# Performance work log

Measured on AMD Instinct MI355X. Metric: run time of the kernel, lower is better.

Reference implementation:

```python
import jax, jax.numpy as jnp
import numpy as np

DIM = 3072
HEADS = 24
HD = 128  # head_dim
RANK = 64
COND = 1024      # (512//8)*(512//8)*16//64
BLOCK = 2048     # main latent tokens
SEQ = BLOCK + COND
NIP = 64         # image_emb tokens
LORA_W = 1.0     # lora_weights[0]
ALPHA_SCALE = 1.0  # network_alpha / rank = 64/64
IP_SCALE = 1.0


def setup_inputs() -> dict:
    key = jax.random.key(0)
    ks = jax.random.split(key, 21)
    d = {}
    d["hidden_states"] = jax.random.normal(ks[0], (1, SEQ, DIM), jnp.float32)
    d["image_emb"] = jax.random.normal(ks[1], (1, NIP, DIM), jnp.float32)
    d["rope_cos"] = jax.random.uniform(ks[2], (SEQ, HD), jnp.float32)
    d["rope_sin"] = jax.random.uniform(ks[3], (SEQ, HD), jnp.float32)
    d["wq"] = jax.random.normal(ks[4], (DIM, DIM), jnp.float32) * 0.02
    d["bq"] = jax.random.normal(ks[5], (DIM,), jnp.float32) * 0.02
    d["wk"] = jax.random.normal(ks[6], (DIM, DIM), jnp.float32) * 0.02
    d["bk"] = jax.random.normal(ks[7], (DIM,), jnp.float32) * 0.02
    d["wv"] = jax.random.normal(ks[8], (DIM, DIM), jnp.float32) * 0.02
    d["bv"] = jax.random.normal(ks[9], (DIM,), jnp.float32) * 0.02
    d["norm_q_w"] = jax.random.uniform(ks[10], (HD,), jnp.float32, 0.5, 1.5)
    d["norm_k_w"] = jax.random.uniform(ks[11], (HD,), jnp.float32, 0.5, 1.5)
    d["q_down"] = jax.random.normal(ks[12], (RANK, DIM), jnp.float32) / RANK
    d["q_up"] = jax.random.normal(ks[13], (DIM, RANK), jnp.float32) * 0.02
    d["k_down"] = jax.random.normal(ks[14], (RANK, DIM), jnp.float32) / RANK
    d["k_up"] = jax.random.normal(ks[15], (DIM, RANK), jnp.float32) * 0.02
    d["v_down"] = jax.random.normal(ks[16], (RANK, DIM), jnp.float32) / RANK
    d["v_up"] = jax.random.normal(ks[17], (DIM, RANK), jnp.float32) * 0.02
    d["wk_ip"] = jax.random.normal(ks[18], (DIM, DIM), jnp.float32) * 0.02
    d["wv_ip"] = jax.random.normal(ks[19], (DIM, DIM), jnp.float32) * 0.02
    return d


def _rmsnorm(x, w, eps):
    v = jnp.mean(jnp.square(x), axis=-1, keepdims=True)
    y = x * jax.lax.rsqrt(v + eps)
    return y if w is None else y * w


def _heads(x, b):  # (B,S,DIM) -> (B,H,S,HD)
    return x.reshape(b, -1, HEADS, HD).transpose(0, 2, 1, 3)


def _rope(x, cos, sin):
    # diffusers apply_rotary_emb, use_real, unbind_dim=-1
    x1 = x[..., 0::2]
    x2 = x[..., 1::2]
    rot = jnp.stack([-x2, x1], axis=-1).reshape(x.shape)
    return x * cos[None, None] + rot * sin[None, None]


def _sdpa(q, k, v, bias=None):
    s = jnp.einsum("bhqd,bhkd->bhqk", q, k) / jnp.sqrt(jnp.float32(q.shape[-1]))
    if bias is not None:
        s = s + bias
    p = jax.nn.softmax(s, axis=-1)
    return jnp.einsum("bhqk,bhkd->bhqd", p, v)


def reference(hidden_states, image_emb, rope_cos, rope_sin,
              wq, bq, wk, bk, wv, bv, norm_q_w, norm_k_w,
              q_down, q_up, k_down, k_up, v_down, v_up, wk_ip, wv_ip):
    B = hidden_states.shape[0]

    # base QKV projections
    q = hidden_states @ wq.T + bq
    k = hidden_states @ wk.T + bk
    v = hidden_states @ wv.T + bv

    # original (pre-LoRA, pre-norm, pre-RoPE) query on the main block for IP attention
    original_query = _heads(hidden_states[:, :BLOCK] @ wq.T + bq, B)

    # masked LoRA add (n_loras=1): only tokens [BLOCK, BLOCK+COND) contribute
    pos = jnp.arange(SEQ)
    tok_mask = ((pos >= BLOCK) & (pos < BLOCK + COND)).astype(hidden_states.dtype)
    hm = hidden_states * tok_mask[None, :, None]
    q = q + LORA_W * ALPHA_SCALE * ((hm @ q_down.T) @ q_up.T)
    k = k + LORA_W * ALPHA_SCALE * ((hm @ k_down.T) @ k_up.T)
    v = v + LORA_W * ALPHA_SCALE * ((hm @ v_down.T) @ v_up.T)

    q = _heads(q, B)
    k = _heads(k, B)
    v = _heads(v, B)

    # per-head RMSNorm (attn.norm_q / attn.norm_k, eps=1e-6 in Flux)
    q = _rmsnorm(q, norm_q_w, 1e-6)
    k = _rmsnorm(k, norm_k_w, 1e-6)

    # IP-adapter cross attention with the original query
    ip_k = _rmsnorm(_heads(image_emb @ wk_ip.T, B), None, 1e-5)
    ip_v = _heads(image_emb @ wv_ip.T, B)
    ip_out = _sdpa(original_query, ip_k, ip_v)  # (B,H,BLOCK,HD)
    ip_out = ip_out.transpose(0, 2, 1, 3).reshape(B, -1, DIM)

    # RoPE on q/k
    q = _rope(q, rope_cos, rope_sin)
    k = _rope(k, rope_cos, rope_sin)

    # attention bias: main-block queries see everything; cond queries only their own block
    m = jnp.ones((SEQ, SEQ), jnp.float32)
    m = m.at[:BLOCK, :].set(0.0)
    m = m.at[BLOCK:BLOCK + COND, BLOCK:BLOCK + COND].set(0.0)
    bias = (m * -1e20)[None, None]

    out = _sdpa(q, k, v, bias)  # (B,H,SEQ,HD)
    out = out.transpose(0, 2, 1, 3).reshape(B, SEQ, DIM)

    main = out[:, :BLOCK, :] + IP_SCALE * ip_out
    return main
```

## Files before the change

### kernel.cpp

```cpp
#include <hip/hip_runtime.h>
#include <stdint.h>

#define DIM 3072
#define HEADS 24
#define HD 128
#define RANKN 64
#define CONDN 1024
#define BLK 2048
#define SEQN 3072
#define NIPN 64

typedef __attribute__((ext_vector_type(8))) short s8v;
typedef __attribute__((ext_vector_type(4))) float fx4;

static __device__ __forceinline__ unsigned short f2bf(float f){
  union{float f; unsigned u;} v; v.f=f;
  unsigned r = v.u + 0x7FFFu + ((v.u>>16)&1u);
  return (unsigned short)(r>>16);
}

#define GL16(g,l) __builtin_amdgcn_global_load_lds((const __attribute__((address_space(1))) void*)(g), (__attribute__((address_space(3))) void*)(l), 16, 0, 0)
#define MFMA(a,b,c) __builtin_amdgcn_mfma_f32_16x16x32_bf16((a),(b),(c),0,0,0)

__global__ __launch_bounds__(256) void cvt_f32_bf16(const float* __restrict__ src,
                                                    unsigned short* __restrict__ dst, int n4){
  int i = blockIdx.x*256 + threadIdx.x;
  if (i < n4){
    float4 v = ((const float4*)src)[i];
    ushort4 o;
    o.x = f2bf(v.x); o.y = f2bf(v.y); o.z = f2bf(v.z); o.w = f2bf(v.w);
    ((ushort4*)dst)[i] = o;
  }
}

__global__ __launch_bounds__(256) void lora_down_g(const unsigned short* __restrict__ A,
                                                   const unsigned short* __restrict__ D0,
                                                   const unsigned short* __restrict__ D1,
                                                   unsigned short* __restrict__ outb){
  __shared__ unsigned short As[128*64];
  __shared__ unsigned short Bs[64*64];
  int tid = threadIdx.x, lane = tid & 63, w = tid >> 6;
  int l15 = lane & 15, l16 = lane >> 4;
  int z = blockIdx.z;
  int m0 = blockIdx.y * 128;
  const unsigned short* Dw = z ? D1 : D0;
  int wr = w * 32;
  fx4 acc[2][4] = {};
  for (int kt = 0; kt < DIM; kt += 64){
    #pragma unroll
    for (int i = 0; i < 4; i++){
      int p = i*256 + tid;
      int row = p >> 3, cc = p & 7;
      int gc = cc ^ (row & 7);
      GL16(A + (size_t)(m0+row)*DIM + kt + gc*8, As + p*8);
    }
    #pragma unroll
    for (int i = 0; i < 2; i++){
      int p = i*256 + tid;
      int row = p >> 3, cc = p & 7;
      int gc = cc ^ (row & 7);
      GL16(Dw + (size_t)row*DIM + kt + gc*8, Bs + p*8);
    }
    __syncthreads();
    #pragma unroll
    for (int kk = 0; kk < 2; kk++){
      s8v af[2], bfr[4];
      #pragma unroll
      for (int t = 0; t < 2; t++){
        int rowa = wr + t*16 + l15;
        int ca = (kk*4 + l16) ^ (rowa & 7);
        af[t] = *(const s8v*)(As + rowa*64 + ca*8);
      }
      #pragma unroll
      for (int t = 0; t < 4; t++){
        int rowb = t*16 + l15;
        int cb = (kk*4 + l16) ^ (rowb & 7);
        bfr[t] = *(const s8v*)(Bs + rowb*64 + cb*8);
      }
      #pragma unroll
      for (int mt = 0; mt < 2; mt++)
        #pragma unroll
        for (int nt = 0; nt < 4; nt++)
          acc[mt][nt] = MFMA(af[mt], bfr[nt], acc[mt][nt]);
    }
    __syncthreads();
  }
  #pragma unroll
  for (int mt = 0; mt < 2; mt++)
    #pragma unroll
    for (int j = 0; j < 4; j++){
      int row = m0 + wr + mt*16 + l16*4 + j;
      #pragma unroll
      for (int nt = 0; nt < 4; nt++){
        int col = nt*16 + l15;
        outb[((size_t)z*CONDN + row)*64 + col] = f2bf(acc[mt][nt][j]);
      }
    }
}

__global__ __launch_bounds__(512, 2) void gemm_256(
    const unsigned short* __restrict__ hs_bf,
    const unsigned short* __restrict__ ie_bf,
    const unsigned short* __restrict__ Wq,
    const unsigned short* __restrict__ Wk,
    const unsigned short* __restrict__ Wv,
    const unsigned short* __restrict__ Wik,
    const unsigned short* __restrict__ Wiv,
    const float* __restrict__ bq, const float* __restrict__ bk, const float* __restrict__ bv,
    const unsigned short* __restrict__ downb,
    const unsigned short* __restrict__ upk,
    const unsigned short* __restrict__ upv,
    float* __restrict__ qb, float* __restrict__ kb, float* __restrict__ vb,
    float* __restrict__ ipk_pre, float* __restrict__ ipv_pre)
{
  __shared__ unsigned short Ab[2][16384];
  __shared__ unsigned short Bb[2][16384];
  int tid = threadIdx.x, lane = tid & 63, w = tid >> 6;
  int wm = w >> 2, wn = w & 3;
  int l15 = lane & 15, l16 = lane >> 4;

  int b = blockIdx.x;
  int id = (b & 7) * 51 + (b >> 3);
  int z, mt, ntile;
  if (id < 96){ z = 0; mt = id / 12; ntile = id % 12; }
  else if (id < 240){ z = 1; int r = id - 96; mt = r / 12; ntile = r % 12; }
  else if (id < 384){ z = 2; int r = id - 240; mt = r / 12; ntile = r % 12; }
  else { z = 3; int r = id - 384; mt = r / 12; ntile = r % 12; }
  const bool is_ip = (z == 3);
  int z2 = is_ip ? mt : 0;
  int m0 = is_ip ? 0 : mt * 256;
  int n0 = ntile * 256;
  const unsigned short* A = is_ip ? ie_bf : hs_bf;
  const unsigned short* B = is_ip ? (z2 ? Wiv : Wik)
                                  : (z == 0 ? Wq : (z == 1 ? Wk : Wv));

  fx4 acc[8][4] = {};
  s8v af[8], bfr[8];

  auto stA = [&](int buf, int half, int kt){
    #pragma unroll
    for (int i = 0; i < 2; i++){
      int p = i*512 + tid;
      int row = p >> 3, cc = p & 7, gc = cc ^ (row & 7);
      int ar = m0 + half*128 + row;
      if (is_ip && ar > 63) ar = 63;
      GL16(A + (size_t)ar*DIM + kt + gc*8, &Ab[buf][half*8192 + p*8]);
    }
  };
  auto stB = [&](int buf, int half, int kt){
    #pragma unroll
    for (int i = 0; i < 2; i++){
      int p = i*512 + tid;
      int row = p >> 3, cc = p & 7, gc = cc ^ (row & 7);
      GL16(B + (size_t)(n0 + half*128 + row)*DIM + kt + gc*8, &Bb[buf][half*8192 + p*8]);
    }
  };
  auto rdA = [&](int buf, int m, int kk)->s8v{
    int rl = m*16 + l15;
    return *(const s8v*)(&Ab[buf][wm*8192 + rl*64 + ((kk*4 + l16) ^ (rl & 7))*8]);
  };
  auto rdB = [&](int buf, int n, int kk)->s8v{
    int rB = wn*64 + n*16 + l15;
    return *(const s8v*)(&Bb[buf][(rB >> 7)*8192 + (rB & 127)*64 + ((kk*4 + l16) ^ (rB & 7))*8]);
  };

  stA(0,0,0); stA(0,1,0); stB(0,0,0); stB(0,1,0);
  asm volatile("s_waitcnt vmcnt(0)" ::: "memory");
  __builtin_amdgcn_s_barrier();

  const int NT = DIM / 64;
  for (int t = 0; t < NT; t++){
    int cur = t & 1, nxt = cur ^ 1;
    int kt1 = (t + 1) * 64;
    bool pf = (t + 1 < NT);

    if (pf){
      stA(nxt, 0, kt1);
      asm volatile("s_waitcnt vmcnt(2)" ::: "memory");
    } else {
      asm volatile("s_waitcnt vmcnt(0)" ::: "memory");
    }
    __builtin_amdgcn_s_barrier();
    #pragma unroll
    for (int m = 0; m < 4; m++){ af[m*2] = rdA(cur,m,0); af[m*2+1] = rdA(cur,m,1); }
    #pragma unroll
    for (int n = 0; n < 2; n++){ bfr[n*2] = rdB(cur,n,0); bfr[n*2+1] = rdB(cur,n,1); }
    __builtin_amdgcn_s_setprio(1);
    #pragma unroll
    for (int m = 0; m < 4; m++)
      #pragma unroll
      for (int n = 0; n < 2; n++){
        acc[m][n] = MFMA(af[m*2],   bfr[n*2],   acc[m][n]);
        acc[m][n] = MFMA(af[m*2+1], bfr[n*2+1], acc[m][n]);
      }
    __builtin_amdgcn_s_setprio(0);
    __builtin_amdgcn_s_barrier();

    if (pf) stA(nxt, 1, kt1);
    #pragma unroll
    for (int n = 2; n < 4; n++){ bfr[n*2] = rdB(cur,n,0); bfr[n*2+1] = rdB(cur,n,1); }
    __builtin_amdgcn_s_setprio(1);
    #pragma unroll
    for (int m = 0; m < 4; m++)
      #pragma unroll
      for (int n = 2; n < 4; n++){
        acc[m][n] = MFMA(af[m*2],   bfr[n*2],   acc[m][n]);
        acc[m][n] = MFMA(af[m*2+1], bfr[n*2+1], acc[m][n]);
      }
    __builtin_amdgcn_s_setprio(0);
    __builtin_amdgcn_s_barrier();

    if (pf) stB(nxt, 0, kt1);
    #pragma unroll
    for (int m = 4; m < 8; m++){ af[(m-4)*2] = rdA(cur,m,0); af[(m-4)*2+1] = rdA(cur,m,1); }
    __builtin_amdgcn_s_setprio(1);
    #pragma unroll
    for (int m = 4; m < 8; m++)
      #pragma unroll
      for (int n = 2; n < 4; n++){
        acc[m][n] = MFMA(af[(m-4)*2],   bfr[n*2],   acc[m][n]);
        acc[m][n] = MFMA(af[(m-4)*2+1], bfr[n*2+1], acc[m][n]);
      }
    __builtin_amdgcn_s_setprio(0);
    __builtin_amdgcn_s_barrier();

    if (pf) stB(nxt, 1, kt1);
    __builtin_amdgcn_s_setprio(1);
    #pragma unroll
    for (int m = 4; m < 8; m++)
      #pragma unroll
      for (int n = 0; n < 2; n++){
        acc[m][n] = MFMA(af[(m-4)*2],   bfr[n*2],   acc[m][n]);
        acc[m][n] = MFMA(af[(m-4)*2+1], bfr[n*2+1], acc[m][n]);
      }
    __builtin_amdgcn_s_setprio(0);
    __builtin_amdgcn_s_barrier();
  }

  if (is_ip){
    float* outp = z2 ? ipv_pre : ipk_pre;
    if (wm == 0){
      #pragma unroll
      for (int m = 0; m < 4; m++)
        #pragma unroll
        for (int j = 0; j < 4; j++){
          int row = m*16 + l16*4 + j;
          #pragma unroll
          for (int n = 0; n < 4; n++)
            outp[(size_t)row*DIM + n0 + wn*64 + n*16 + l15] = acc[m][n][j];
        }
    }
    return;
  }

  if (z >= 1 && m0 >= BLK){
    const unsigned short* dwn = downb + (size_t)(z-1)*CONDN*64 + (size_t)(m0 - BLK)*64;
    const unsigned short* up  = (z == 1) ? upk : upv;
    #pragma unroll
    for (int i = 0; i < 4; i++){
      int p = i*512 + tid;
      int row = p >> 3, cc = p & 7, gc = cc ^ (row & 7);
      GL16(dwn + (size_t)row*64 + gc*8, &Ab[0][p*8]);
      GL16(up + (size_t)(n0 + row)*64 + gc*8, &Bb[0][p*8]);
    }
    asm volatile("s_waitcnt vmcnt(0)" ::: "memory");
    __builtin_amdgcn_s_barrier();
    #pragma unroll
    for (int kk = 0; kk < 2; kk++){
      s8v aL[8], bL[4];
      #pragma unroll
      for (int m = 0; m < 8; m++){
        int rA = wm*128 + m*16 + l15;
        aL[m] = *(const s8v*)(&Ab[0][rA*64 + ((kk*4 + l16) ^ (rA & 7))*8]);
      }
      #pragma unroll
      for (int n = 0; n < 4; n++){
        int rB = wn*64 + n*16 + l15;
        bL[n] = *(const s8v*)(&Bb[0][rB*64 + ((kk*4 + l16) ^ (rB & 7))*8]);
      }
      #pragma unroll
      for (int m = 0; m < 8; m++)
        #pragma unroll
        for (int n = 0; n < 4; n++)
          acc[m][n] = MFMA(aL[m], bL[n], acc[m][n]);
    }
  }

  {
    const float* bias = z == 0 ? bq : (z == 1 ? bk : bv);
    float* C = z == 0 ? qb : (z == 1 ? kb : vb);
    float bv4[4];
    #pragma unroll
    for (int n = 0; n < 4; n++) bv4[n] = bias[n0 + wn*64 + n*16 + l15];
    #pragma unroll
    for (int m = 0; m < 8; m++)
      #pragma unroll
      for (int j = 0; j < 4; j++){
        int row = m0 + wm*128 + m*16 + l16*4 + j;
        float* crow = C + (size_t)row*DIM;
        #pragma unroll
        for (int n = 0; n < 4; n++)
          crow[n0 + wn*64 + n*16 + l15] = acc[m][n][j] + bv4[n];
      }
  }
}

__global__ __launch_bounds__(256) void norm_rope(const float* __restrict__ src,
                                                 unsigned short* __restrict__ dst,
                                                 const float* __restrict__ wt,
                                                 const float* __restrict__ rc,
                                                 const float* __restrict__ rs,
                                                 int S, float qscale){
  int tid = threadIdx.x, lane = tid & 63, w = tid >> 6;
  int r = blockIdx.x*4 + w;
  int pos = r % S, h = r / S;
  const float* x = src + (size_t)pos*DIM + h*HD;
  float2 xv = *(const float2*)(x + 2*lane);
  float ss = xv.x*xv.x + xv.y*xv.y;
  #pragma unroll
  for (int o = 1; o < 64; o <<= 1) ss += __shfl_xor(ss, o);
  float rr = rsqrtf(ss*(1.f/128.f) + 1e-6f);
  float y0 = xv.x*rr*wt[2*lane], y1 = xv.y*rr*wt[2*lane+1];
  float2 cv = *(const float2*)(rc + (size_t)pos*HD + 2*lane);
  float2 sv = *(const float2*)(rs + (size_t)pos*HD + 2*lane);
  float o0 = (y0*cv.x - y1*sv.x)*qscale;
  float o1 = (y1*cv.y + y0*sv.y)*qscale;
  ushort2 ov; ov.x = f2bf(o0); ov.y = f2bf(o1);
  *(ushort2*)(dst + ((size_t)h*S + pos)*HD + 2*lane) = ov;
}

__global__ __launch_bounds__(256) void ipk_norm_bf(const float* __restrict__ src,
                                                   unsigned short* __restrict__ dst){
  int tid = threadIdx.x, lane = tid & 63, w = tid >> 6;
  int r = blockIdx.x*4 + w;
  int pos = r / HEADS, h = r % HEADS;
  const float* x = src + (size_t)pos*DIM + h*HD;
  float2 xv = *(const float2*)(x + 2*lane);
  float ss = xv.x*xv.x + xv.y*xv.y;
  #pragma unroll
  for (int o = 1; o < 64; o <<= 1) ss += __shfl_xor(ss, o);
  float rr = rsqrtf(ss*(1.f/128.f) + 1e-5f);
  ushort2 ov; ov.x = f2bf(xv.x*rr); ov.y = f2bf(xv.y*rr);
  *(ushort2*)(dst + ((size_t)h*NIPN + pos)*HD + 2*lane) = ov;
}

__global__ __launch_bounds__(256) void ipv_transpose(const float* __restrict__ ipv,
                                                     unsigned short* __restrict__ vt){
  int h = blockIdx.x, tid = threadIdx.x;
  #pragma unroll
  for (int i = 0; i < 32; i++){
    int idx = i*256 + tid;
    int d = idx >> 6, key = idx & 63;
    vt[((size_t)h*HD + d)*64 + key] = f2bf(ipv[(size_t)key*DIM + h*HD + d]);
  }
}

__global__ __launch_bounds__(256) void v_transpose(const float* __restrict__ v,
                                                   unsigned short* __restrict__ Vt){
  __shared__ float t[64][129];
  int h = blockIdx.y, p0 = blockIdx.x*64, tid = threadIdx.x;
  int dcol = tid & 127, prow2 = tid >> 7;
  #pragma unroll
  for (int i = 0; i < 32; i++){
    int pos = i*2 + prow2;
    t[pos][dcol] = v[(size_t)(p0+pos)*DIM + h*HD + dcol];
  }
  __syncthreads();
  int pos = tid & 63, dbase = tid >> 6;
  #pragma unroll
  for (int i = 0; i < 32; i++){
    int d = i*4 + dbase;
    Vt[((size_t)h*HD + d)*SEQN + p0 + pos] = f2bf(t[pos][d]);
  }
}

__global__ __launch_bounds__(256) void ip_attn_m(const float* __restrict__ qb,
                                                 const unsigned short* __restrict__ ipk_bf,
                                                 const unsigned short* __restrict__ ipv_t,
                                                 float* __restrict__ out){
  __shared__ unsigned short Ks[64*HD];
  __shared__ unsigned short Vs[HD*64];
  __shared__ unsigned short Ps[4][16*64];
  int tid = threadIdx.x, lane = tid & 63, w = tid >> 6;
  int l15 = lane & 15, l16 = lane >> 4;
  int h = blockIdx.y;
  int q0 = blockIdx.x*64 + w*16;
  const unsigned short* Kh = ipk_bf + (size_t)h*NIPN*HD;
  const unsigned short* Vh = ipv_t + (size_t)h*HD*NIPN;

  #pragma unroll
  for (int i = 0; i < 4; i++){
    int p = i*256 + tid;
    int row = p >> 4, cc = p & 15;
    int gc = cc ^ (row & 7);
    GL16(Kh + (size_t)row*HD + gc*8, Ks + p*8);
  }
  #pragma unroll
  for (int i = 0; i < 4; i++){
    int p = i*256 + tid;
    int row = p >> 3, cc = p & 7;
    int gc = cc ^ (row & 7);
    GL16(Vh + (size_t)row*64 + gc*8, Vs + p*8);
  }

  s8v qf[4];
  #pragma unroll
  for (int kf = 0; kf < 4; kf++){
    const float* qp = qb + (size_t)(q0 + l15)*DIM + h*HD + kf*32 + l16*8;
    float4 a = *(const float4*)qp;
    float4 b = *(const float4*)(qp + 4);
    s8v f;
    f[0]=(short)f2bf(a.x); f[1]=(short)f2bf(a.y); f[2]=(short)f2bf(a.z); f[3]=(short)f2bf(a.w);
    f[4]=(short)f2bf(b.x); f[5]=(short)f2bf(b.y); f[6]=(short)f2bf(b.z); f[7]=(short)f2bf(b.w);
    qf[kf] = f;
  }
  __syncthreads();

  fx4 s[4] = {};
  #pragma unroll
  for (int ct = 0; ct < 4; ct++){
    #pragma unroll
    for (int kk = 0; kk < 4; kk++){
      int row = ct*16 + l15;
      int c = (kk*4 + l16) ^ (row & 7);
      s8v b = *(const s8v*)(Ks + row*HD + c*8);
      s[ct] = MFMA(qf[kk], b, s[ct]);
    }
  }
  const float SC = 0.08838834764831845f;
  float lrow[4];
  #pragma unroll
  for (int j = 0; j < 4; j++){
    #pragma unroll
    for (int ct = 0; ct < 4; ct++) s[ct][j] *= SC;
    float v = fmaxf(fmaxf(s[0][j], s[1][j]), fmaxf(s[2][j], s[3][j]));
    #pragma unroll
    for (int o2 = 1; o2 < 16; o2 <<= 1) v = fmaxf(v, __shfl_xor(v, o2));
    float sum = 0.f;
    #pragma unroll
    for (int ct = 0; ct < 4; ct++){
      float p = __expf(s[ct][j] - v);
      s[ct][j] = p;
      sum += p;
    }
    #pragma unroll
    for (int o2 = 1; o2 < 16; o2 <<= 1) sum += __shfl_xor(sum, o2);
    lrow[j] = sum;
  }

  #pragma unroll
  for (int ct = 0; ct < 4; ct++)
    #pragma unroll
    for (int j = 0; j < 4; j++){
      int row = l16*4 + j;
      int cidx = ct*16 + l15;
      Ps[w][row*64 + (((cidx>>3) ^ (row&7))<<3) + (cidx&7)] = f2bf(s[ct][j]);
    }
  asm volatile("s_waitcnt lgkmcnt(0)" ::: "memory");
  s8v pa[2];
  #pragma unroll
  for (int kk = 0; kk < 2; kk++){
    int c = (kk*4 + l16) ^ (l15 & 7);
    pa[kk] = *(const s8v*)(&Ps[w][l15*64 + c*8]);
  }
  fx4 o[8] = {};
  #pragma unroll
  for (int nt = 0; nt < 8; nt++){
    #pragma unroll
    for (int kk = 0; kk < 2; kk++){
      int row = nt*16 + l15;
      int c = (kk*4 + l16) ^ (row & 7);
      s8v bv = *(const s8v*)(Vs + row*64 + c*8);
      o[nt] = MFMA(pa[kk], bv, o[nt]);
    }
  }
  #pragma unroll
  for (int nt = 0; nt < 8; nt++)
    #pragma unroll
    for (int j = 0; j < 4; j++){
      int row = q0 + l16*4 + j;
      int d = nt*16 + l15;
      out[(size_t)row*DIM + h*HD + d] = o[nt][j] / lrow[j];
    }
}

#define QB 128
#define KVB 64
#define PSTR 72
__global__ __launch_bounds__(512, 4) void flash_attn_split(const unsigned short* __restrict__ Qn,
                                                           const unsigned short* __restrict__ Kn,
                                                           const unsigned short* __restrict__ Vt,
                                                           float* __restrict__ po0,
                                                           float* __restrict__ po1,
                                                           float* __restrict__ pm,
                                                           float* __restrict__ pl){
  __shared__ unsigned short Ks[KVB*HD];
  __shared__ unsigned short Vs[HD*KVB];
  __shared__ unsigned short Ps[8][16*PSTR];
  int tid = threadIdx.x, lane = tid & 63, w = tid >> 6;
  int l15 = lane & 15, l16 = lane >> 4;
  int b = blockIdx.x;
  int swz = (b & 7) * 96 + (b >> 3);
  int sp = swz / 384;
  int rem = swz - sp*384;
  int h = rem >> 4;
  int qt = rem & 15;
  int q0 = qt*QB + w*16;
  const unsigned short* Qh = Qn + (size_t)h*BLK*HD;
  const unsigned short* Kh = Kn + (size_t)h*SEQN*HD;
  const unsigned short* Vh = Vt + (size_t)h*HD*SEQN;
  const int kvbase = sp * (SEQN/2);
  const int NT = (SEQN/2) / KVB;

  s8v qf[4];
  #pragma unroll
  for (int kf = 0; kf < 4; kf++)
    qf[kf] = *(const s8v*)(Qh + (size_t)(q0 + l15)*HD + kf*32 + l16*8);

  fx4 o[8] = {};
  float mrow[4], lrow[4];
  #pragma unroll
  for (int j = 0; j < 4; j++){ mrow[j] = -1e30f; lrow[j] = 0.f; }

  for (int t = 0; t < NT; t++){
    int kv0 = kvbase + t*KVB;
    #pragma unroll
    for (int i = 0; i < 2; i++){
      int p = i*512 + tid;
      int row = p >> 4, cc = p & 15;
      int gc = cc ^ (row & 7);
      GL16(Kh + (size_t)(kv0+row)*HD + gc*8, Ks + p*8);
    }
    #pragma unroll
    for (int i = 0; i < 2; i++){
      int p = i*512 + tid;
      int row = p >> 3, cc = p & 7;
      int gc = cc ^ (row & 7);
      GL16(Vh + (size_t)row*SEQN + kv0 + gc*8, Vs + p*8);
    }
    __syncthreads();

    fx4 s[4] = {};
    #pragma unroll
    for (int ct = 0; ct < 4; ct++){
      #pragma unroll
      for (int kk = 0; kk < 4; kk++){
        int row = ct*16 + l15;
        int c = (kk*4 + l16) ^ (row & 7);
        s8v bb = *(const s8v*)(Ks + row*HD + c*8);
        s[ct] = MFMA(qf[kk], bb, s[ct]);
      }
    }
    float pmax[4], rssum[4];
    #pragma unroll
    for (int j = 0; j < 4; j++){
      float v = fmaxf(fmaxf(s[0][j], s[1][j]), fmaxf(s[2][j], s[3][j]));
      #pragma unroll
      for (int o2 = 1; o2 < 16; o2 <<= 1) v = fmaxf(v, __shfl_xor(v, o2));
      pmax[j] = v;
      rssum[j] = 0.f;
    }
    float need = 0.f;
    #pragma unroll
    for (int j = 0; j < 4; j++) need = fmaxf(need, pmax[j] - mrow[j]);
    if (__any(need > 8.f)){
      float alpha[4];
      #pragma unroll
      for (int j = 0; j < 4; j++){
        float mnew = fmaxf(mrow[j], pmax[j]);
        alpha[j] = __expf(mrow[j] - mnew);
        mrow[j] = mnew;
      }
      #pragma unroll
      for (int nt = 0; nt < 8; nt++)
        #pragma unroll
        for (int j = 0; j < 4; j++) o[nt][j] *= alpha[j];
      #pragma unroll
      for (int j = 0; j < 4; j++) lrow[j] *= alpha[j];
    }
    #pragma unroll
    for (int ct = 0; ct < 4; ct++)
      #pragma unroll
      for (int j = 0; j < 4; j++){
        float p = __expf(s[ct][j] - mrow[j]);
        s[ct][j] = p;
        rssum[j] += p;
      }
    #pragma unroll
    for (int j = 0; j < 4; j++){
      #pragma unroll
      for (int o2 = 1; o2 < 16; o2 <<= 1) rssum[j] += __shfl_xor(rssum[j], o2);
      lrow[j] += rssum[j];
    }

    #pragma unroll
    for (int ct = 0; ct < 4; ct++)
      #pragma unroll
      for (int j = 0; j < 4; j++){
        int row = l16*4 + j;
        int cidx = ct*16 + l15;
        Ps[w][row*PSTR + cidx] = f2bf(s[ct][j]);
      }
    asm volatile("s_waitcnt lgkmcnt(0)" ::: "memory");
    s8v pa[2];
    #pragma unroll
    for (int kk = 0; kk < 2; kk++)
      pa[kk] = *(const s8v*)(&Ps[w][l15*PSTR + (kk*4 + l16)*8]);
    #pragma unroll
    for (int nt = 0; nt < 8; nt++){
      #pragma unroll
      for (int kk = 0; kk < 2; kk++){
        int row = nt*16 + l15;
        int c = (kk*4 + l16) ^ (row & 7);
        s8v bvv = *(const s8v*)(Vs + row*KVB + c*8);
        o[nt] = MFMA(pa[kk], bvv, o[nt]);
      }
    }
    __syncthreads();
  }

  float* pop = sp ? po1 : po0;
  #pragma unroll
  for (int nt = 0; nt < 8; nt++)
    #pragma unroll
    for (int j = 0; j < 4; j++){
      int row = q0 + l16*4 + j;
      int d = nt*16 + l15;
      pop[((size_t)h*BLK + row)*HD + d] = o[nt][j];
    }
  if (l15 == 0){
    #pragma unroll
    for (int j = 0; j < 4; j++){
      int row = q0 + l16*4 + j;
      pm[(size_t)sp*HEADS*BLK + h*BLK + row] = mrow[j];
      pl[(size_t)sp*HEADS*BLK + h*BLK + row] = lrow[j];
    }
  }
}

__global__ __launch_bounds__(256) void flash_merge(const float* __restrict__ po0,
                                                   const float* __restrict__ po1,
                                                   const float* __restrict__ pm,
                                                   const float* __restrict__ pl,
                                                   float* __restrict__ out){
  int tid = threadIdx.x, lane = tid & 63, w = tid >> 6;
  int r = blockIdx.x*4 + w;
  int h = r >> 11, pos = r & 2047;
  float m0 = pm[r], m1 = pm[HEADS*BLK + r];
  float l0 = pl[r], l1 = pl[HEADS*BLK + r];
  float mx = fmaxf(m0, m1);
  float a0 = __expf(m0 - mx), a1 = __expf(m1 - mx);
  float li = 1.f / (l0*a0 + l1*a1);
  float s0 = a0*li, s1 = a1*li;
  size_t base = ((size_t)h*BLK + pos)*HD + 2*lane;
  float2 x0 = *(const float2*)(po0 + base);
  float2 x1 = *(const float2*)(po1 + base);
  float* op = out + (size_t)pos*DIM + h*HD + 2*lane;
  float2 cv = *(const float2*)op;
  cv.x += x0.x*s0 + x1.x*s1;
  cv.y += x0.y*s0 + x1.y*s1;
  *(float2*)op = cv;
}

extern "C" void kernel_launch(void* const* d_in, const int* in_sizes, int n_in,
                              void* d_out, int out_size, void* d_ws, size_t ws_size,
                              hipStream_t stream){
  (void)in_sizes; (void)n_in; (void)out_size;
  const float* hs       = (const float*)d_in[0];
  const float* image_emb= (const float*)d_in[1];
  const float* rope_cos = (const float*)d_in[2];
  const float* rope_sin = (const float*)d_in[3];
  const float* wq = (const float*)d_in[4];
  const float* bq = (const float*)d_in[5];
  const float* wk = (const float*)d_in[6];
  const float* bk = (const float*)d_in[7];
  const float* wv = (const float*)d_in[8];
  const float* bv = (const float*)d_in[9];
  const float* norm_q_w = (const float*)d_in[10];
  const float* norm_k_w = (const float*)d_in[11];
  const float* k_down = (const float*)d_in[14];
  const float* k_up   = (const float*)d_in[15];
  const float* v_down = (const float*)d_in[16];
  const float* v_up   = (const float*)d_in[17];
  const float* wk_ip  = (const float*)d_in[18];
  const float* wv_ip  = (const float*)d_in[19];
  float* out = (float*)d_out;

  char* ws = (char*)d_ws;
  size_t off = 0;
  auto alloc = [&](size_t bytes){ void* p = ws + off; off += (bytes + 255) & ~(size_t)255; return p; };
  unsigned short* hs_bf = (unsigned short*)alloc((size_t)SEQN*DIM*2);
  unsigned short* ie_bf = (unsigned short*)alloc((size_t)NIPN*DIM*2);
  unsigned short* w_bf[5];
  for (int i = 0; i < 5; i++) w_bf[i] = (unsigned short*)alloc((size_t)DIM*DIM*2);
  unsigned short* lw_bf[4];
  for (int i = 0; i < 4; i++) lw_bf[i] = (unsigned short*)alloc((size_t)RANKN*DIM*2);
  unsigned short* downb = (unsigned short*)alloc((size_t)2*CONDN*RANKN*2);
  float* qb = (float*)alloc((size_t)BLK*DIM*4);
  float* kb = (float*)alloc((size_t)SEQN*DIM*4);
  float* vb = (float*)alloc((size_t)SEQN*DIM*4);
  float* ipk_pre = (float*)alloc((size_t)NIPN*DIM*4);
  float* ipv_pre = (float*)alloc((size_t)NIPN*DIM*4);
  unsigned short* ipk_bf = (unsigned short*)alloc((size_t)HEADS*NIPN*HD*2);
  unsigned short* ipv_t  = (unsigned short*)alloc((size_t)HEADS*HD*NIPN*2);
  float* pm  = (float*)alloc((size_t)2*HEADS*BLK*4);
  float* pl  = (float*)alloc((size_t)2*HEADS*BLK*4);
  if (off > ws_size) return;

  unsigned short* Qn = w_bf[0];
  unsigned short* Kn = w_bf[1];
  unsigned short* Vt = w_bf[2];
  float* po0 = qb;
  float* po1 = kb;

  int n4;
  n4 = SEQN*DIM/4;
  cvt_f32_bf16<<<(n4+255)/256, 256, 0, stream>>>(hs, hs_bf, n4);
  n4 = NIPN*DIM/4;
  cvt_f32_bf16<<<(n4+255)/256, 256, 0, stream>>>(image_emb, ie_bf, n4);

  n4 = DIM*DIM/4;
  cvt_f32_bf16<<<(n4+255)/256, 256, 0, stream>>>(wq, w_bf[0], n4);
  cvt_f32_bf16<<<(n4+255)/256, 256, 0, stream>>>(wk, w_bf[1], n4);
  cvt_f32_bf16<<<(n4+255)/256, 256, 0, stream>>>(wv, w_bf[2], n4);
  cvt_f32_bf16<<<(n4+255)/256, 256, 0, stream>>>(wk_ip, w_bf[3], n4);
  cvt_f32_bf16<<<(n4+255)/256, 256, 0, stream>>>(wv_ip, w_bf[4], n4);

  n4 = RANKN*DIM/4;
  cvt_f32_bf16<<<(n4+255)/256, 256, 0, stream>>>(k_down, lw_bf[0], n4);
  cvt_f32_bf16<<<(n4+255)/256, 256, 0, stream>>>(v_down, lw_bf[1], n4);
  cvt_f32_bf16<<<(n4+255)/256, 256, 0, stream>>>(k_up,   lw_bf[2], n4);
  cvt_f32_bf16<<<(n4+255)/256, 256, 0, stream>>>(v_up,   lw_bf[3], n4);

  lora_down_g<<<dim3(1, CONDN/128, 2), 256, 0, stream>>>(hs_bf + (size_t)BLK*DIM,
      lw_bf[0], lw_bf[1], downb);

  gemm_256<<<408, 512, 0, stream>>>(hs_bf, ie_bf,
      w_bf[0], w_bf[1], w_bf[2], w_bf[3], w_bf[4],
      bq, bk, bv, downb, lw_bf[2], lw_bf[3],
      qb, kb, vb, ipk_pre, ipv_pre);

  ipk_norm_bf<<<(NIPN*HEADS)/4, 256, 0, stream>>>(ipk_pre, ipk_bf);
  ipv_transpose<<<HEADS, 256, 0, stream>>>(ipv_pre, ipv_t);

  const float SC = 0.08838834764831845f;
  norm_rope<<<(BLK*HEADS)/4, 256, 0, stream>>>(qb, Qn, norm_q_w, rope_cos, rope_sin, BLK, SC);
  norm_rope<<<(SEQN*HEADS)/4, 256, 0, stream>>>(kb, Kn, norm_k_w, rope_cos, rope_sin, SEQN, 1.0f);
  v_transpose<<<dim3(SEQN/64, HEADS), 256, 0, stream>>>(vb, Vt);

  ip_attn_m<<<dim3(BLK/64, HEADS), 256, 0, stream>>>(qb, ipk_bf, ipv_t, out);
  flash_attn_split<<<768, 512, 0, stream>>>(Qn, Kn, Vt, po0, po1, pm, pl);
  flash_merge<<<(HEADS*BLK)/4, 256, 0, stream>>>(po0, po1, pm, pl, out);
}
```

Baseline: 576.6 us.

## Store projected Q/K/V as bf16 and simplify GEMM prefetch pipeline

The big projection GEMM now writes Q, K and V as bf16 instead of fp32. The downstream norm_rope, v_transpose and ip_attn kernels read bf16 directly, which roughly halves the traffic on these intermediates and removes the repeated conversions. The GEMM main loop now issues all next-tile loads at the top of each iteration and drops three of the four intra-iteration barriers, trading finer-grained overlap for less synchronization. Because qb and kb no longer hold fp32, the split attention partials get their own fp32 workspace buffers, and Q/K/V are rounded to bf16 once before the norms.

```diff
diff --git a/kernel.cpp b/kernel.cpp
--- a/kernel.cpp
+++ b/kernel.cpp
@@ -17,6 +17,10 @@
   union{float f; unsigned u;} v; v.f=f;
   unsigned r = v.u + 0x7FFFu + ((v.u>>16)&1u);
   return (unsigned short)(r>>16);
+}
+static __device__ __forceinline__ float bf2f(unsigned short b){
+  union{unsigned u; float f;} v; v.u = ((unsigned)b) << 16;
+  return v.f;
 }
 
 #define GL16(g,l) __builtin_amdgcn_global_load_lds((const __attribute__((address_space(1))) void*)(g), (__attribute__((address_space(3))) void*)(l), 16, 0, 0)
@@ -110,7 +114,7 @@
     const unsigned short* __restrict__ downb,
     const unsigned short* __restrict__ upk,
     const unsigned short* __restrict__ upv,
-    float* __restrict__ qb, float* __restrict__ kb, float* __restrict__ vb,
+    unsigned short* __restrict__ qb, unsigned short* __restrict__ kb, unsigned short* __restrict__ vb,
     float* __restrict__ ipk_pre, float* __restrict__ ipv_pre)
 {
   __shared__ unsigned short Ab[2][16384];
@@ -165,22 +169,21 @@
   };
 
   stA(0,0,0); stA(0,1,0); stB(0,0,0); stB(0,1,0);
-  asm volatile("s_waitcnt vmcnt(0)" ::: "memory");
-  __builtin_amdgcn_s_barrier();
 
   const int NT = DIM / 64;
   for (int t = 0; t < NT; t++){
     int cur = t & 1, nxt = cur ^ 1;
-    int kt1 = (t + 1) * 64;
     bool pf = (t + 1 < NT);
-
     if (pf){
-      stA(nxt, 0, kt1);
-      asm volatile("s_waitcnt vmcnt(2)" ::: "memory");
+      int kt1 = (t + 1) * 64;
+      stA(nxt, 0, kt1); stA(nxt, 1, kt1);
+      stB(nxt, 0, kt1); stB(nxt, 1, kt1);
+      asm volatile("s_waitcnt vmcnt(8)" ::: "memory");
     } else {
       asm volatile("s_waitcnt vmcnt(0)" ::: "memory");
     }
     __builtin_amdgcn_s_barrier();
+
     #pragma unroll
     for (int m = 0; m < 4; m++){ af[m*2] = rdA(cur,m,0); af[m*2+1] = rdA(cur,m,1); }
     #pragma unroll
@@ -194,9 +197,6 @@
         acc[m][n] = MFMA(af[m*2+1], bfr[n*2+1], acc[m][n]);
       }
     __builtin_amdgcn_s_setprio(0);
-    __builtin_amdgcn_s_barrier();
-
-    if (pf) stA(nxt, 1, kt1);
     #pragma unroll
     for (int n = 2; n < 4; n++){ bfr[n*2] = rdB(cur,n,0); bfr[n*2+1] = rdB(cur,n,1); }
     __builtin_amdgcn_s_setprio(1);
@@ -208,9 +208,6 @@
         acc[m][n] = MFMA(af[m*2+1], bfr[n*2+1], acc[m][n]);
       }
     __builtin_amdgcn_s_setprio(0);
-    __builtin_amdgcn_s_barrier();
-
-    if (pf) stB(nxt, 0, kt1);
     #pragma unroll
     for (int m = 4; m < 8; m++){ af[(m-4)*2] = rdA(cur,m,0); af[(m-4)*2+1] = rdA(cur,m,1); }
     __builtin_amdgcn_s_setprio(1);
@@ -221,11 +218,6 @@
         acc[m][n] = MFMA(af[(m-4)*2],   bfr[n*2],   acc[m][n]);
         acc[m][n] = MFMA(af[(m-4)*2+1], bfr[n*2+1], acc[m][n]);
       }
-    __builtin_amdgcn_s_setprio(0);
-    __builtin_amdgcn_s_barrier();
-
-    if (pf) stB(nxt, 1, kt1);
-    __builtin_amdgcn_s_setprio(1);
     #pragma unroll
     for (int m = 4; m < 8; m++)
       #pragma unroll
@@ -288,7 +280,7 @@
 
   {
     const float* bias = z == 0 ? bq : (z == 1 ? bk : bv);
-    float* C = z == 0 ? qb : (z == 1 ? kb : vb);
+    unsigned short* C = z == 0 ? qb : (z == 1 ? kb : vb);
     float bv4[4];
     #pragma unroll
     for (int n = 0; n < 4; n++) bv4[n] = bias[n0 + wn*64 + n*16 + l15];
@@ -297,15 +289,15 @@
       #pragma unroll
       for (int j = 0; j < 4; j++){
         int row = m0 + wm*128 + m*16 + l16*4 + j;
-        float* crow = C + (size_t)row*DIM;
+        unsigned short* crow = C + (size_t)row*DIM;
         #pragma unroll
         for (int n = 0; n < 4; n++)
-          crow[n0 + wn*64 + n*16 + l15] = acc[m][n][j] + bv4[n];
-      }
-  }
-}
-
-__global__ __launch_bounds__(256) void norm_rope(const float* __restrict__ src,
+          crow[n0 + wn*64 + n*16 + l15] = f2bf(acc[m][n][j] + bv4[n]);
+      }
+  }
+}
+
+__global__ __launch_bounds__(256) void norm_rope(const unsigned short* __restrict__ src,
                                                  unsigned short* __restrict__ dst,
                                                  const float* __restrict__ wt,
                                                  const float* __restrict__ rc,
@@ -314,13 +306,14 @@
   int tid = threadIdx.x, lane = tid & 63, w = tid >> 6;
   int r = blockIdx.x*4 + w;
   int pos = r % S, h = r / S;
-  const float* x = src + (size_t)pos*DIM + h*HD;
-  float2 xv = *(const float2*)(x + 2*lane);
-  float ss = xv.x*xv.x + xv.y*xv.y;
+  const unsigned short* x = src + (size_t)pos*DIM + h*HD;
+  ushort2 xv2 = *(const ushort2*)(x + 2*lane);
+  float x0 = bf2f(xv2.x), x1 = bf2f(xv2.y);
+  float ss = x0*x0 + x1*x1;
   #pragma unroll
   for (int o = 1; o < 64; o <<= 1) ss += __shfl_xor(ss, o);
   float rr = rsqrtf(ss*(1.f/128.f) + 1e-6f);
-  float y0 = xv.x*rr*wt[2*lane], y1 = xv.y*rr*wt[2*lane+1];
+  float y0 = x0*rr*wt[2*lane], y1 = x1*rr*wt[2*lane+1];
   float2 cv = *(const float2*)(rc + (size_t)pos*HD + 2*lane);
   float2 sv = *(const float2*)(rs + (size_t)pos*HD + 2*lane);
   float o0 = (y0*cv.x - y1*sv.x)*qscale;
@@ -355,9 +348,9 @@
   }
 }
 
-__global__ __launch_bounds__(256) void v_transpose(const float* __restrict__ v,
+__global__ __launch_bounds__(256) void v_transpose(const unsigned short* __restrict__ v,
                                                    unsigned short* __restrict__ Vt){
-  __shared__ float t[64][129];
+  __shared__ unsigned short t[64][137];
   int h = blockIdx.y, p0 = blockIdx.x*64, tid = threadIdx.x;
   int dcol = tid & 127, prow2 = tid >> 7;
   #pragma unroll
@@ -370,11 +363,11 @@
   #pragma unroll
   for (int i = 0; i < 32; i++){
     int d = i*4 + dbase;
-    Vt[((size_t)h*HD + d)*SEQN + p0 + pos] = f2bf(t[pos][d]);
-  }
-}
-
-__global__ __launch_bounds__(256) void ip_attn_m(const float* __restrict__ qb,
+    Vt[((size_t)h*HD + d)*SEQN + p0 + pos] = t[pos][d];
+  }
+}
+
+__global__ __launch_bounds__(256) void ip_attn_m(const unsigned short* __restrict__ qb,
                                                  const unsigned short* __restrict__ ipk_bf,
                                                  const unsigned short* __restrict__ ipv_t,
                                                  float* __restrict__ out){
@@ -405,15 +398,8 @@
 
   s8v qf[4];
   #pragma unroll
-  for (int kf = 0; kf < 4; kf++){
-    const float* qp = qb + (size_t)(q0 + l15)*DIM + h*HD + kf*32 + l16*8;
-    float4 a = *(const float4*)qp;
-    float4 b = *(const float4*)(qp + 4);
-    s8v f;
-    f[0]=(short)f2bf(a.x); f[1]=(short)f2bf(a.y); f[2]=(short)f2bf(a.z); f[3]=(short)f2bf(a.w);
-    f[4]=(short)f2bf(b.x); f[5]=(short)f2bf(b.y); f[6]=(short)f2bf(b.z); f[7]=(short)f2bf(b.w);
-    qf[kf] = f;
-  }
+  for (int kf = 0; kf < 4; kf++)
+    qf[kf] = *(const s8v*)(qb + (size_t)(q0 + l15)*DIM + h*HD + kf*32 + l16*8);
   __syncthreads();
 
   fx4 s[4] = {};
@@ -696,13 +682,15 @@
   unsigned short* lw_bf[4];
   for (int i = 0; i < 4; i++) lw_bf[i] = (unsigned short*)alloc((size_t)RANKN*DIM*2);
   unsigned short* downb = (unsigned short*)alloc((size_t)2*CONDN*RANKN*2);
-  float* qb = (float*)alloc((size_t)BLK*DIM*4);
-  float* kb = (float*)alloc((size_t)SEQN*DIM*4);
-  float* vb = (float*)alloc((size_t)SEQN*DIM*4);
+  unsigned short* qb = (unsigned short*)alloc((size_t)BLK*DIM*2);
+  unsigned short* kb = (unsigned short*)alloc((size_t)SEQN*DIM*2);
+  unsigned short* vb = (unsigned short*)alloc((size_t)SEQN*DIM*2);
   float* ipk_pre = (float*)alloc((size_t)NIPN*DIM*4);
   float* ipv_pre = (float*)alloc((size_t)NIPN*DIM*4);
   unsigned short* ipk_bf = (unsigned short*)alloc((size_t)HEADS*NIPN*HD*2);
   unsigned short* ipv_t  = (unsigned short*)alloc((size_t)HEADS*HD*NIPN*2);
+  float* po0 = (float*)alloc((size_t)HEADS*BLK*HD*4);
+  float* po1 = (float*)alloc((size_t)HEADS*BLK*HD*4);
   float* pm  = (float*)alloc((size_t)2*HEADS*BLK*4);
   float* pl  = (float*)alloc((size_t)2*HEADS*BLK*4);
   if (off > ws_size) return;
@@ -710,8 +698,6 @@
   unsigned short* Qn = w_bf[0];
   unsigned short* Kn = w_bf[1];
   unsigned short* Vt = w_bf[2];
-  float* po0 = qb;
-  float* po1 = kb;
 
   int n4;
   n4 = SEQN*DIM/4;
```

Result: faster. 547.8 us (-5.0%).
